# Performance work log

Measured on AMD Instinct MI355X. Metric: run time of the kernel, lower is better.

## Reference

```python
import jax, jax.numpy as jnp
import numpy as np

N = 50000      # nodes
E = 800000     # edges (avg degree 16)
IN, H, C = 128, 256, 47


def _linear_init(key, nin, nout):
    bound = 1.0 / np.sqrt(nin)
    kw, kb = jax.random.split(key)
    w = jax.random.uniform(kw, (nin, nout), jnp.float32, -bound, bound)
    b = jax.random.uniform(kb, (nout,), jnp.float32, -bound, bound)
    return w, b


def setup_inputs() -> dict:
    key = jax.random.key(0)
    ks = jax.random.split(key, 9)
    x = jax.random.normal(ks[0], (N, IN), jnp.float32)
    row = jax.random.randint(ks[1], (E,), 0, N)   # dst node of each edge
    col = jax.random.randint(ks[2], (E,), 0, N)   # src node of each edge
    y = jax.random.randint(ks[3], (N,), 0, C)
    train_mask = jax.random.randint(ks[4], (N,), 0, 2).astype(jnp.bool_)
    w1n, b1n = _linear_init(ks[5], IN, H)
    w1s, b1s = _linear_init(ks[6], IN, H)
    w2n, b2n = _linear_init(ks[7], H, C)
    w2s, b2s = _linear_init(ks[8], H, C)
    return {"x": x, "row": row, "col": col, "y": y, "train_mask": train_mask,
            "w1n": w1n, "b1n": b1n, "w1s": w1s, "b1s": b1s,
            "w2n": w2n, "b2n": b2n, "w2s": w2s, "b2s": b2s}


def _mean_aggr(h, row, col):
    # sparse adjacency matmul with reduce='mean': gather src feats, scatter-mean to dst
    s = jax.ops.segment_sum(h[col], row, num_segments=N)          # [N, d]
    deg = jax.ops.segment_sum(jnp.ones((E,), h.dtype), row, num_segments=N)
    return jnp.where(deg[:, None] > 0, s / jnp.maximum(deg, 1.0)[:, None], 0.0)


def reference(x, row, col, y, train_mask,
              w1n, b1n, w1s, b1s, w2n, b2n, w2s, b2s):
    # dropout in eval mode -> identity
    h = x
    # layer 1: SAGE = linear(mean_aggr(h)) + linear(h), then ReLU
    a = _mean_aggr(h, row, col)
    h1 = jax.nn.relu((a @ w1n + b1n) + (h @ w1s + b1s))           # [N, H]
    # layer 2 (output): SAGE then log_softmax
    a2 = _mean_aggr(h1, row, col)
    logits = (a2 @ w2n + b2n) + (h1 @ w2s + b2s)                  # [N, C]
    logp = jax.nn.log_softmax(logits, axis=1)
    nll = -jnp.take_along_axis(logp, y[:, None], axis=1)[:, 0]    # [N]
    m = train_mask.astype(logits.dtype)
    # nll_loss mean over train nodes; single chunk -> loss / num_chunks == loss
    loss = jnp.sum(nll * m) / jnp.maximum(jnp.sum(m), 1.0)
    return loss
```

## Files before the change

### kernel.cpp

```cpp
#include <hip/hip_runtime.h>
#include <math.h>

#define NN 50000
#define EE 800000
#define DIN 128
#define HH 256
#define CC 47
#define LK2 264
#define GS_BLOCKS 2048

typedef short bf16x8 __attribute__((ext_vector_type(8)));
typedef float f32x4 __attribute__((ext_vector_type(4)));
typedef float f32x2 __attribute__((ext_vector_type(2)));

static __device__ __forceinline__ unsigned short f2bf(float f) {
    unsigned u = __float_as_uint(f);
    u = u + 0x7fff + ((u >> 16) & 1);
    return (unsigned short)(u >> 16);
}
static __device__ __forceinline__ float bflo(unsigned u) { return __uint_as_float(u << 16); }
static __device__ __forceinline__ float bfhi(unsigned u) { return __uint_as_float(u & 0xffff0000u); }

__global__ __launch_bounds__(256) void prep_kernel(
    const float* __restrict__ x, const int* __restrict__ row,
    const int* __restrict__ col, const int* __restrict__ msk,
    const float* __restrict__ w1n, const float* __restrict__ w1s,
    const float* __restrict__ b1n, const float* __restrict__ b1s,
    const float* __restrict__ w2n, const float* __restrict__ w2s,
    int* __restrict__ cnt, unsigned short* __restrict__ bucket,
    unsigned* __restrict__ xq, unsigned* __restrict__ ab,
    unsigned short* __restrict__ WB1, unsigned short* __restrict__ WB2,
    float* __restrict__ bias1, int* __restrict__ mcount, int* __restrict__ mlist)
{
    int t = blockIdx.x * 256 + threadIdx.x;
    if (t < EE) {
        int r = row[t];
        int pos = atomicAdd(&cnt[r], 1);
        if (pos < 64) bucket[r * 64 + pos] = (unsigned short)col[t];
    }
    if (t < NN && msk[t]) {
        int p = atomicAdd(mcount, 1);
        mlist[p] = t;
    }
    if (t < NN * 32) {
        int i = t >> 5, c = t & 31;
        float4 v = *(const float4*)&x[(size_t)i * DIN + c * 4];
        int p = __builtin_amdgcn_cvt_pk_fp8_f32(v.x, v.y, 0, false);
        p = __builtin_amdgcn_cvt_pk_fp8_f32(v.z, v.w, p, true);
        xq[(size_t)i * 32 + c] = (unsigned)p;
        ab[(size_t)i * 128 + 64 + 2 * c]     = (unsigned)f2bf(v.x) | ((unsigned)f2bf(v.y) << 16);
        ab[(size_t)i * 128 + 64 + 2 * c + 1] = (unsigned)f2bf(v.z) | ((unsigned)f2bf(v.w) << 16);
    }
    if (t < 65536) {
        int k = t >> 8, n = t & 255;
        float v = (k < 128) ? w1n[k * HH + n] : w1s[(k - 128) * HH + n];
        WB1[n * 256 + k] = f2bf(v);
    } else if (t < 65536 + 24576) {
        int q = t - 65536;
        int k = q / 96, n = q % 96;
        float v;
        if (n < 48) v = (n < CC) ? w2n[k * CC + n] : 0.f;
        else { int m = n - 48; v = (m < CC) ? w2s[k * CC + m] : 0.f; }
        WB2[n * 256 + k] = f2bf(v);
    } else if (t < 65536 + 24576 + 256) {
        int n = t - 65536 - 24576;
        bias1[n] = b1n[n] + b1s[n];
    }
}

__global__ __launch_bounds__(256) void agg1(const unsigned* __restrict__ xq,
                                            const int* __restrict__ cnt,
                                            const unsigned short* __restrict__ bucket,
                                            unsigned* __restrict__ ab,
                                            float* __restrict__ inv) {
    int wave = threadIdx.x >> 6, lane = threadIdx.x & 63;
    const int h = lane >> 5, hl = lane & 31;
    const int W = gridDim.x * 4;
    for (int i = blockIdx.x * 4 + wave; i < NN; i += W) {
        int e = cnt[i];
        float dvs = fmaxf((float)e, 1.0f);
        if (e > 64) e = 64;
        float A0=0,A1=0,A2=0,A3=0, B0=0,B1=0,B2=0,B3=0;
        float C0=0,C1=0,C2=0,C3=0, D0=0,D1=0,D2=0,D3=0;
        if (e > 0) {
            int myidx = bucket[i * 64 + min(lane, e - 1)];
            int j = 0;
            for (; j + 16 <= e; j += 16) {
                int n0 = __shfl(myidx, j + h);
                int n1 = __shfl(myidx, j + 2 + h);
                int n2 = __shfl(myidx, j + 4 + h);
                int n3 = __shfl(myidx, j + 6 + h);
                int n4 = __shfl(myidx, j + 8 + h);
                int n5 = __shfl(myidx, j + 10 + h);
                int n6 = __shfl(myidx, j + 12 + h);
                int n7 = __shfl(myidx, j + 14 + h);
                unsigned u0 = xq[(size_t)n0 * 32 + hl];
                unsigned u1 = xq[(size_t)n1 * 32 + hl];
                unsigned u2 = xq[(size_t)n2 * 32 + hl];
                unsigned u3 = xq[(size_t)n3 * 32 + hl];
                unsigned u4 = xq[(size_t)n4 * 32 + hl];
                unsigned u5 = xq[(size_t)n5 * 32 + hl];
                unsigned u6 = xq[(size_t)n6 * 32 + hl];
                unsigned u7 = xq[(size_t)n7 * 32 + hl];
                f32x2 l0 = __builtin_amdgcn_cvt_pk_f32_fp8(u0, false);
                f32x2 h0 = __builtin_amdgcn_cvt_pk_f32_fp8(u0, true);
                f32x2 l1 = __builtin_amdgcn_cvt_pk_f32_fp8(u1, false);
                f32x2 h1 = __builtin_amdgcn_cvt_pk_f32_fp8(u1, true);
                f32x2 l2 = __builtin_amdgcn_cvt_pk_f32_fp8(u2, false);
                f32x2 h2 = __builtin_amdgcn_cvt_pk_f32_fp8(u2, true);
                f32x2 l3 = __builtin_amdgcn_cvt_pk_f32_fp8(u3, false);
                f32x2 h3 = __builtin_amdgcn_cvt_pk_f32_fp8(u3, true);
                A0 += l0.x; A1 += l0.y; A2 += h0.x; A3 += h0.y;
                B0 += l1.x; B1 += l1.y; B2 += h1.x; B3 += h1.y;
                C0 += l2.x; C1 += l2.y; C2 += h2.x; C3 += h2.y;
                D0 += l3.x; D1 += l3.y; D2 += h3.x; D3 += h3.y;
                f32x2 l4 = __builtin_amdgcn_cvt_pk_f32_fp8(u4, false);
                f32x2 h4 = __builtin_amdgcn_cvt_pk_f32_fp8(u4, true);
                f32x2 l5 = __builtin_amdgcn_cvt_pk_f32_fp8(u5, false);
                f32x2 h5 = __builtin_amdgcn_cvt_pk_f32_fp8(u5, true);
                f32x2 l6 = __builtin_amdgcn_cvt_pk_f32_fp8(u6, false);
                f32x2 h6 = __builtin_amdgcn_cvt_pk_f32_fp8(u6, true);
                f32x2 l7 = __builtin_amdgcn_cvt_pk_f32_fp8(u7, false);
                f32x2 h7 = __builtin_amdgcn_cvt_pk_f32_fp8(u7, true);
                A0 += l4.x; A1 += l4.y; A2 += h4.x; A3 += h4.y;
                B0 += l5.x; B1 += l5.y; B2 += h5.x; B3 += h5.y;
                C0 += l6.x; C1 += l6.y; C2 += h6.x; C3 += h6.y;
                D0 += l7.x; D1 += l7.y; D2 += h7.x; D3 += h7.y;
            }
            for (; j + 8 <= e; j += 8) {
                int n0 = __shfl(myidx, j + h);
                int n1 = __shfl(myidx, j + 2 + h);
                int n2 = __shfl(myidx, j + 4 + h);
                int n3 = __shfl(myidx, j + 6 + h);
                unsigned u0 = xq[(size_t)n0 * 32 + hl];
                unsigned u1 = xq[(size_t)n1 * 32 + hl];
                unsigned u2 = xq[(size_t)n2 * 32 + hl];
                unsigned u3 = xq[(size_t)n3 * 32 + hl];
                f32x2 l0 = __builtin_amdgcn_cvt_pk_f32_fp8(u0, false);
                f32x2 h0 = __builtin_amdgcn_cvt_pk_f32_fp8(u0, true);
                f32x2 l1 = __builtin_amdgcn_cvt_pk_f32_fp8(u1, false);
                f32x2 h1 = __builtin_amdgcn_cvt_pk_f32_fp8(u1, true);
                f32x2 l2 = __builtin_amdgcn_cvt_pk_f32_fp8(u2, false);
                f32x2 h2 = __builtin_amdgcn_cvt_pk_f32_fp8(u2, true);
                f32x2 l3 = __builtin_amdgcn_cvt_pk_f32_fp8(u3, false);
                f32x2 h3 = __builtin_amdgcn_cvt_pk_f32_fp8(u3, true);
                A0 += l0.x; A1 += l0.y; A2 += h0.x; A3 += h0.y;
                B0 += l1.x; B1 += l1.y; B2 += h1.x; B3 += h1.y;
                C0 += l2.x; C1 += l2.y; C2 += h2.x; C3 += h2.y;
                D0 += l3.x; D1 += l3.y; D2 += h3.x; D3 += h3.y;
            }
            for (; j < e; j += 2) {
                int src = j + h;
                int n = __shfl(myidx, min(src, e - 1));
                unsigned u = xq[(size_t)n * 32 + hl];
                if (src >= e) u = 0u;
                f32x2 lo = __builtin_amdgcn_cvt_pk_f32_fp8(u, false);
                f32x2 hi = __builtin_amdgcn_cvt_pk_f32_fp8(u, true);
                A0 += lo.x; A1 += lo.y; A2 += hi.x; A3 += hi.y;
            }
        }
        float s0 = (A0 + B0) + (C0 + D0);
        float s1 = (A1 + B1) + (C1 + D1);
        float s2 = (A2 + B2) + (C2 + D2);
        float s3 = (A3 + B3) + (C3 + D3);
        s0 += __shfl_xor(s0, 32); s1 += __shfl_xor(s1, 32);
        s2 += __shfl_xor(s2, 32); s3 += __shfl_xor(s3, 32);
        if (h == 0) {
            float sc = 1.0f / dvs;
            if (hl == 0) inv[i] = sc;
            unsigned d0 = (unsigned)f2bf(s0 * sc) | ((unsigned)f2bf(s1 * sc) << 16);
            unsigned d1 = (unsigned)f2bf(s2 * sc) | ((unsigned)f2bf(s3 * sc) << 16);
            *(uint2*)&ab[(size_t)i * 128 + 2 * hl] = make_uint2(d0, d1);
        }
    }
}

__global__ __launch_bounds__(256) void gemm12_fused(
    const unsigned short* __restrict__ AB,
    const unsigned short* __restrict__ WB1, const unsigned short* __restrict__ WB2,
    const float* __restrict__ bias1,
    const float* __restrict__ b2n, const float* __restrict__ b2s,
    unsigned* __restrict__ znb, float* __restrict__ zsb)
{
    __shared__ unsigned short sA[32 * LK2];
    __shared__ unsigned short sB[32 * LK2];
    __shared__ unsigned short sH[32 * LK2];
    const int tid = threadIdx.x;
    const int i0 = blockIdx.x * 32;
    const int wv = tid >> 6, lane = tid & 63;
    const int g = lane >> 4, l16 = lane & 15;
    const int m0 = (wv & 1) * 16, q0 = (wv >> 1) * 16;

#pragma unroll
    for (int l = 0; l < 4; ++l) {
        int c = tid + l * 256;
        int r = c >> 5, c8 = (c & 31) * 8;
        int gi = i0 + r;
        int4 v = make_int4(0, 0, 0, 0);
        if (gi < NN) v = *(const int4*)&AB[(size_t)gi * 256 + c8];
        *(int4*)&sA[r * LK2 + c8] = v;
    }

    for (int n0 = 0; n0 < 8; ++n0) {
#pragma unroll
        for (int l = 0; l < 4; ++l) {
            int c = tid + l * 256;
            int r = c >> 5, c8 = (c & 31) * 8;
            *(int4*)&sB[r * LK2 + c8] = *(const int4*)&WB1[(size_t)(n0 * 32 + r) * 256 + c8];
        }
        __syncthreads();
        f32x4 p0 = {}, p1 = {}, p2 = {}, p3 = {};
        {
            const unsigned short* ar = &sA[(m0 + l16) * LK2 + g * 8];
            const unsigned short* br = &sB[(q0 + l16) * LK2 + g * 8];
            p0 = __builtin_amdgcn_mfma_f32_16x16x32_bf16(*(const bf16x8*)(ar +   0), *(const bf16x8*)(br +   0), p0, 0, 0, 0);
            p1 = __builtin_amdgcn_mfma_f32_16x16x32_bf16(*(const bf16x8*)(ar +  32), *(const bf16x8*)(br +  32), p1, 0, 0, 0);
            p2 = __builtin_amdgcn_mfma_f32_16x16x32_bf16(*(const bf16x8*)(ar +  64), *(const bf16x8*)(br +  64), p2, 0, 0, 0);
            p3 = __builtin_amdgcn_mfma_f32_16x16x32_bf16(*(const bf16x8*)(ar +  96), *(const bf16x8*)(br +  96), p3, 0, 0, 0);
            p0 = __builtin_amdgcn_mfma_f32_16x16x32_bf16(*(const bf16x8*)(ar + 128), *(const bf16x8*)(br + 128), p0, 0, 0, 0);
            p1 = __builtin_amdgcn_mfma_f32_16x16x32_bf16(*(const bf16x8*)(ar + 160), *(const bf16x8*)(br + 160), p1, 0, 0, 0);
            p2 = __builtin_amdgcn_mfma_f32_16x16x32_bf16(*(const bf16x8*)(ar + 192), *(const bf16x8*)(br + 192), p2, 0, 0, 0);
            p3 = __builtin_amdgcn_mfma_f32_16x16x32_bf16(*(const bf16x8*)(ar + 224), *(const bf16x8*)(br + 224), p3, 0, 0, 0);
        }
        f32x4 acc = (p0 + p1) + (p2 + p3);
        int colh = n0 * 32 + q0 + l16;
        float bi = bias1[colh];
#pragma unroll
        for (int r = 0; r < 4; ++r)
            sH[(m0 + g * 4 + r) * LK2 + colh] = f2bf(fmaxf(acc[r] + bi, 0.f));
        __syncthreads();
    }

    for (int m = 0; m < 3; ++m) {
#pragma unroll
        for (int l = 0; l < 4; ++l) {
            int c = tid + l * 256;
            int r = c >> 5, c8 = (c & 31) * 8;
            *(int4*)&sB[r * LK2 + c8] = *(const int4*)&WB2[(size_t)(m * 32 + r) * 256 + c8];
        }
        __syncthreads();
        f32x4 p0 = {}, p1 = {}, p2 = {}, p3 = {};
        {
            const unsigned short* ar = &sH[(m0 + l16) * LK2 + g * 8];
            const unsigned short* br = &sB[(q0 + l16) * LK2 + g * 8];
            p0 = __builtin_amdgcn_mfma_f32_16x16x32_bf16(*(const bf16x8*)(ar +   0), *(const bf16x8*)(br +   0), p0, 0, 0, 0);
            p1 = __builtin_amdgcn_mfma_f32_16x16x32_bf16(*(const bf16x8*)(ar +  32), *(const bf16x8*)(br +  32), p1, 0, 0, 0);
            p2 = __builtin_amdgcn_mfma_f32_16x16x32_bf16(*(const bf16x8*)(ar +  64), *(const bf16x8*)(br +  64), p2, 0, 0, 0);
            p3 = __builtin_amdgcn_mfma_f32_16x16x32_bf16(*(const bf16x8*)(ar +  96), *(const bf16x8*)(br +  96), p3, 0, 0, 0);
            p0 = __builtin_amdgcn_mfma_f32_16x16x32_bf16(*(const bf16x8*)(ar + 128), *(const bf16x8*)(br + 128), p0, 0, 0, 0);
            p1 = __builtin_amdgcn_mfma_f32_16x16x32_bf16(*(const bf16x8*)(ar + 160), *(const bf16x8*)(br + 160), p1, 0, 0, 0);
            p2 = __builtin_amdgcn_mfma_f32_16x16x32_bf16(*(const bf16x8*)(ar + 192), *(const bf16x8*)(br + 192), p2, 0, 0, 0);
            p3 = __builtin_amdgcn_mfma_f32_16x16x32_bf16(*(const bf16x8*)(ar + 224), *(const bf16x8*)(br + 224), p3, 0, 0, 0);
        }
        f32x4 acc = (p0 + p1) + (p2 + p3);
        int c = m * 32 + q0 + l16;
        if (c < 48) {
#pragma unroll
            for (int r = 0; r < 4; ++r) {
                int gi = i0 + m0 + g * 4 + r;
                float v = acc[r];
                float vp = __shfl_down(v, 1);
                if (((l16 & 1) == 0) && gi < NN)
                    znb[(size_t)gi * 24 + (c >> 1)] =
                        (unsigned)f2bf(v) | ((unsigned)f2bf(vp) << 16);
            }
        } else {
            int cz = c - 48;
            float bias = (cz < CC) ? (b2n[cz] + b2s[cz]) : 0.f;
#pragma unroll
            for (int r = 0; r < 4; ++r) {
                int gi = i0 + m0 + g * 4 + r;
                if (gi < NN) zsb[(size_t)gi * 48 + cz] = acc[r] + bias;
            }
        }
        __syncthreads();
    }
}

__global__ __launch_bounds__(256) void loss_kernel(
    const unsigned* __restrict__ znb, const float* __restrict__ zsb,
    const int* __restrict__ cnt, const unsigned short* __restrict__ bucket,
    const float* __restrict__ inv, const int* __restrict__ y,
    const int* __restrict__ mcount, const int* __restrict__ mlist,
    float* __restrict__ accum)
{
    __shared__ float red[16];
    const int tid = threadIdx.x;
    const int wave = tid >> 6, lane = tid & 63;
    const int half = lane >> 5, hl = lane & 31;
    const int h32 = lane & 32;
    const bool act = hl < 24;
    const int dw = act ? hl : 0;
    const int W = gridDim.x * 8;
    const int M = mcount[0];
    float num = 0.f, den = 0.f;

    for (int p = (blockIdx.x * 4 + wave) * 2 + half; p < M; p += W) {
        int i = mlist[p];
        int e = cnt[i];
        if (e > 64) e = 64;
        float plo[8] = {}, phi[8] = {};
        for (int base = 0; base < e; base += 32) {
            int c2 = min(32, e - base);
            int myidx = bucket[i * 64 + min(base + hl, e - 1)];
            int j = 0;
            for (; j + 8 <= c2; j += 8) {
                unsigned uu[8];
#pragma unroll
                for (int k = 0; k < 8; ++k) {
                    int n = __shfl(myidx, h32 + j + k);
                    uu[k] = znb[(size_t)n * 24 + dw];
                }
#pragma unroll
                for (int k = 0; k < 8; ++k) {
                    plo[k] += bflo(uu[k]); phi[k] += bfhi(uu[k]);
                }
            }
            for (; j + 4 <= c2; j += 4) {
                unsigned uu[4];
#pragma unroll
                for (int k = 0; k < 4; ++k) {
                    int n = __shfl(myidx, h32 + j + k);
                    uu[k] = znb[(size_t)n * 24 + dw];
                }
#pragma unroll
                for (int k = 0; k < 4; ++k) {
                    plo[k] += bflo(uu[k]); phi[k] += bfhi(uu[k]);
                }
            }
            for (; j < c2; ++j) {
                int n = __shfl(myidx, h32 + j);
                unsigned u = znb[(size_t)n * 24 + dw];
                plo[0] += bflo(u); phi[0] += bfhi(u);
            }
        }
        float alo = ((plo[0] + plo[1]) + (plo[2] + plo[3])) +
                    ((plo[4] + plo[5]) + (plo[6] + plo[7]));
        float ahi = ((phi[0] + phi[1]) + (phi[2] + phi[3])) +
                    ((phi[4] + phi[5]) + (phi[6] + phi[7]));

        float sc = inv[i];
        float llo = -1e30f, lhi = -1e30f;
        if (act) {
            float2 zs = *(const float2*)&zsb[(size_t)i * 48 + 2 * hl];
            llo = alo * sc + zs.x;
            lhi = ahi * sc + zs.y;
        }
        if (hl == 23) lhi = -1e30f;
        float mx = fmaxf(llo, lhi);
#pragma unroll
        for (int off = 16; off >= 1; off >>= 1)
            mx = fmaxf(mx, __shfl_xor(mx, off));
        float sm = act ? (__expf(llo - mx) + __expf(lhi - mx)) : 0.f;
#pragma unroll
        for (int off = 16; off >= 1; off >>= 1)
            sm += __shfl_xor(sm, off);
        float lse = mx + __logf(sm);
        int yi = y[i];
        float gl = __shfl(llo, h32 + (yi >> 1));
        float gh = __shfl(lhi, h32 + (yi >> 1));
        float ly = (yi & 1) ? gh : gl;
        if (hl == 0) { num += lse - ly; den += 1.f; }
    }
    if (hl == 0) {
        red[wave * 4 + half * 2]     = num;
        red[wave * 4 + half * 2 + 1] = den;
    }
    __syncthreads();
    if (tid == 0) {
        float n = 0.f, d = 0.f;
#pragma unroll
        for (int k = 0; k < 16; k += 2) { n += red[k]; d += red[k + 1]; }
        atomicAdd(&accum[0], n);
        atomicAdd(&accum[1], d);
    }
}

__global__ void finalize_kernel(const float* __restrict__ accum, float* __restrict__ out) {
    out[0] = accum[0] / fmaxf(accum[1], 1.0f);
}

extern "C" void kernel_launch(void* const* d_in, const int* in_sizes, int n_in,
                              void* d_out, int out_size, void* d_ws, size_t ws_size,
                              hipStream_t stream) {
    const float* x   = (const float*)d_in[0];
    const int*   row = (const int*)d_in[1];
    const int*   col = (const int*)d_in[2];
    const int*   y   = (const int*)d_in[3];
    const int*   msk = (const int*)d_in[4];
    const float* w1n = (const float*)d_in[5];
    const float* b1n = (const float*)d_in[6];
    const float* w1s = (const float*)d_in[7];
    const float* b1s = (const float*)d_in[8];
    const float* w2n = (const float*)d_in[9];
    const float* b2n = (const float*)d_in[10];
    const float* w2s = (const float*)d_in[11];
    const float* b2s = (const float*)d_in[12];
    float* out = (float*)d_out;

    float* ws      = (float*)d_ws;
    float* accum   = ws;
    int*   mcount  = (int*)(ws + 32);
    int*   cnt     = (int*)(ws + 64);
    unsigned short* bucket = (unsigned short*)(cnt + 50048);
    unsigned* xq   = (unsigned*)(bucket + 3200000);
    unsigned* ab   = xq + (size_t)NN * 32;
    unsigned* znb  = ab + (size_t)NN * 128;
    float* zsb     = (float*)(znb + (size_t)NN * 24);
    unsigned short* WB1 = (unsigned short*)(zsb + (size_t)NN * 48);
    unsigned short* WB2 = WB1 + 65536;
    float* bias1   = (float*)(WB2 + 24576);
    int*   mlist   = (int*)(bias1 + 256);
    float* inv     = (float*)(mlist + 50048);

    (void)hipMemsetAsync(accum, 0, (64 + 50048) * sizeof(float), stream);

    prep_kernel<<<(NN * 32 + 255) / 256, 256, 0, stream>>>(
        x, row, col, msk, w1n, w1s, b1n, b1s, w2n, w2s,
        cnt, bucket, xq, ab, WB1, WB2, bias1, mcount, mlist);

    agg1<<<GS_BLOCKS, 256, 0, stream>>>(xq, cnt, bucket, ab, inv);

    gemm12_fused<<<(NN + 31) / 32, 256, 0, stream>>>(
        (const unsigned short*)ab, WB1, WB2, bias1, b2n, b2s, znb, zsb);

    loss_kernel<<<GS_BLOCKS, 256, 0, stream>>>(
        znb, zsb, cnt, bucket, inv, y, mcount, mlist, accum);

    finalize_kernel<<<1, 1, 0, stream>>>(accum, out);
}
```

Baseline: 255.2 us.

## Store layer-2 neighbor logits in fp8 and restructure loss gather per node pairs

The layer-2 neighbor projection is stored as fp8 (16 dwords per node, 64 bytes) instead of bf16 (24 dwords), which shrinks the gather traffic in the loss kernel. The loss kernel now has each half-wave process two fixed consecutive nodes and check the mask inline, dropping the atomic-built masked node list and the stored inverse-degree array. Each half-wave splits into two edge groups of 16 lanes, each lane handling four classes, with a cross-group shuffle reduction. The cost is fp8 rounding error in the aggregated logits, plus idle work on unmasked nodes.

```diff
diff --git a/kernel.cpp b/kernel.cpp
--- a/kernel.cpp
+++ b/kernel.cpp
@@ -8,6 +8,7 @@
 #define CC 47
 #define LK2 264
 #define GS_BLOCKS 2048
+#define LOSS_BLOCKS 3136
 
 typedef short bf16x8 __attribute__((ext_vector_type(8)));
 typedef float f32x4 __attribute__((ext_vector_type(4)));
@@ -18,19 +19,17 @@
     u = u + 0x7fff + ((u >> 16) & 1);
     return (unsigned short)(u >> 16);
 }
-static __device__ __forceinline__ float bflo(unsigned u) { return __uint_as_float(u << 16); }
-static __device__ __forceinline__ float bfhi(unsigned u) { return __uint_as_float(u & 0xffff0000u); }
 
 __global__ __launch_bounds__(256) void prep_kernel(
     const float* __restrict__ x, const int* __restrict__ row,
-    const int* __restrict__ col, const int* __restrict__ msk,
+    const int* __restrict__ col,
     const float* __restrict__ w1n, const float* __restrict__ w1s,
     const float* __restrict__ b1n, const float* __restrict__ b1s,
     const float* __restrict__ w2n, const float* __restrict__ w2s,
     int* __restrict__ cnt, unsigned short* __restrict__ bucket,
     unsigned* __restrict__ xq, unsigned* __restrict__ ab,
     unsigned short* __restrict__ WB1, unsigned short* __restrict__ WB2,
-    float* __restrict__ bias1, int* __restrict__ mcount, int* __restrict__ mlist)
+    float* __restrict__ bias1, unsigned* __restrict__ znq)
 {
     int t = blockIdx.x * 256 + threadIdx.x;
     if (t < EE) {
@@ -38,9 +37,8 @@
         int pos = atomicAdd(&cnt[r], 1);
         if (pos < 64) bucket[r * 64 + pos] = (unsigned short)col[t];
     }
-    if (t < NN && msk[t]) {
-        int p = atomicAdd(mcount, 1);
-        mlist[p] = t;
+    if (t < NN) {
+        *(uint4*)&znq[(size_t)t * 16 + 12] = make_uint4(0u, 0u, 0u, 0u);
     }
     if (t < NN * 32) {
         int i = t >> 5, c = t & 31;
@@ -71,8 +69,7 @@
 __global__ __launch_bounds__(256) void agg1(const unsigned* __restrict__ xq,
                                             const int* __restrict__ cnt,
                                             const unsigned short* __restrict__ bucket,
-                                            unsigned* __restrict__ ab,
-                                            float* __restrict__ inv) {
+                                            unsigned* __restrict__ ab) {
     int wave = threadIdx.x >> 6, lane = threadIdx.x & 63;
     const int h = lane >> 5, hl = lane & 31;
     const int W = gridDim.x * 4;
@@ -167,7 +164,6 @@
         s2 += __shfl_xor(s2, 32); s3 += __shfl_xor(s3, 32);
         if (h == 0) {
             float sc = 1.0f / dvs;
-            if (hl == 0) inv[i] = sc;
             unsigned d0 = (unsigned)f2bf(s0 * sc) | ((unsigned)f2bf(s1 * sc) << 16);
             unsigned d1 = (unsigned)f2bf(s2 * sc) | ((unsigned)f2bf(s3 * sc) << 16);
             *(uint2*)&ab[(size_t)i * 128 + 2 * hl] = make_uint2(d0, d1);
@@ -180,7 +176,7 @@
     const unsigned short* __restrict__ WB1, const unsigned short* __restrict__ WB2,
     const float* __restrict__ bias1,
     const float* __restrict__ b2n, const float* __restrict__ b2s,
-    unsigned* __restrict__ znb, float* __restrict__ zsb)
+    unsigned* __restrict__ znq, float* __restrict__ zsb)
 {
     __shared__ unsigned short sA[32 * LK2];
     __shared__ unsigned short sB[32 * LK2];
@@ -259,10 +255,14 @@
             for (int r = 0; r < 4; ++r) {
                 int gi = i0 + m0 + g * 4 + r;
                 float v = acc[r];
-                float vp = __shfl_down(v, 1);
-                if (((l16 & 1) == 0) && gi < NN)
-                    znb[(size_t)gi * 24 + (c >> 1)] =
-                        (unsigned)f2bf(v) | ((unsigned)f2bf(vp) << 16);
+                float v1 = __shfl_down(v, 1);
+                float v2 = __shfl_down(v, 2);
+                float v3 = __shfl_down(v, 3);
+                if (((l16 & 3) == 0) && gi < NN) {
+                    int pk = __builtin_amdgcn_cvt_pk_fp8_f32(v, v1, 0, false);
+                    pk = __builtin_amdgcn_cvt_pk_fp8_f32(v2, v3, pk, true);
+                    znq[(size_t)gi * 16 + (c >> 2)] = (unsigned)pk;
+                }
             }
         } else {
             int cz = c - 48;
@@ -278,10 +278,9 @@
 }
 
 __global__ __launch_bounds__(256) void loss_kernel(
-    const unsigned* __restrict__ znb, const float* __restrict__ zsb,
-    const int* __restrict__ cnt, const unsigned short* __restrict__ bucket,
-    const float* __restrict__ inv, const int* __restrict__ y,
-    const int* __restrict__ mcount, const int* __restrict__ mlist,
+    const unsigned* __restrict__ znq, const float* __restrict__ zsb,
+    const int* __restrict__ msk, const int* __restrict__ cnt,
+    const unsigned short* __restrict__ bucket, const int* __restrict__ y,
     float* __restrict__ accum)
 {
     __shared__ float red[16];
@@ -289,79 +288,112 @@
     const int wave = tid >> 6, lane = tid & 63;
     const int half = lane >> 5, hl = lane & 31;
     const int h32 = lane & 32;
-    const bool act = hl < 24;
-    const int dw = act ? hl : 0;
-    const int W = gridDim.x * 8;
-    const int M = mcount[0];
+    const int eg = hl >> 4, dwl = hl & 15;
+    const int hw = (blockIdx.x * 4 + wave) * 2 + half;
+    const int base = hw * 2;
     float num = 0.f, den = 0.f;
 
-    for (int p = (blockIdx.x * 4 + wave) * 2 + half; p < M; p += W) {
-        int i = mlist[p];
-        int e = cnt[i];
-        if (e > 64) e = 64;
-        float plo[8] = {}, phi[8] = {};
-        for (int base = 0; base < e; base += 32) {
-            int c2 = min(32, e - base);
-            int myidx = bucket[i * 64 + min(base + hl, e - 1)];
+    int mk2 = 0, c2v = 0, y2 = 0;
+    if (hl < 2 && base + hl < NN) {
+        mk2 = msk[base + hl];
+        c2v = cnt[base + hl];
+        y2  = y[base + hl];
+    }
+    int midx[2];
+#pragma unroll
+    for (int k = 0; k < 2; ++k) {
+        int mkk = __shfl(mk2, h32 + k);
+        int ck  = __shfl(c2v, h32 + k);
+        int ek  = min(ck, 64);
+        midx[k] = 0;
+        if (mkk && ek > 0)
+            midx[k] = bucket[(size_t)(base + k) * 64 + min(hl, ek - 1)];
+    }
+
+#pragma unroll
+    for (int k = 0; k < 2; ++k) {
+        int i = base + k;
+        if (i >= NN) break;
+        int mkk = __shfl(mk2, h32 + k);
+        if (!mkk) continue;
+        int c = __shfl(c2v, h32 + k);
+        int e = min(c, 64);
+        float sc = 1.0f / fmaxf((float)c, 1.0f);
+
+        int dwm = min(dwl, 11);
+        float4 zs = *(const float4*)&zsb[(size_t)i * 48 + 4 * dwm];
+
+        float p0 = 0.f, p1 = 0.f, p2 = 0.f, p3 = 0.f;
+        int mi = midx[k];
+        for (int b = 0; b < e; b += 32) {
+            int cc = min(32, e - b);
+            if (b) mi = bucket[(size_t)i * 64 + min(b + hl, e - 1)];
             int j = 0;
-            for (; j + 8 <= c2; j += 8) {
+            for (; j + 16 <= cc; j += 16) {
                 unsigned uu[8];
 #pragma unroll
-                for (int k = 0; k < 8; ++k) {
-                    int n = __shfl(myidx, h32 + j + k);
-                    uu[k] = znb[(size_t)n * 24 + dw];
+                for (int q = 0; q < 8; ++q) {
+                    int n = __shfl(mi, h32 + j + 2 * q + eg);
+                    uu[q] = znq[(size_t)n * 16 + dwl];
                 }
 #pragma unroll
-                for (int k = 0; k < 8; ++k) {
-                    plo[k] += bflo(uu[k]); phi[k] += bfhi(uu[k]);
+                for (int q = 0; q < 8; ++q) {
+                    f32x2 lo = __builtin_amdgcn_cvt_pk_f32_fp8(uu[q], false);
+                    f32x2 hi = __builtin_amdgcn_cvt_pk_f32_fp8(uu[q], true);
+                    p0 += lo.x; p1 += lo.y; p2 += hi.x; p3 += hi.y;
                 }
             }
-            for (; j + 4 <= c2; j += 4) {
+            for (; j + 8 <= cc; j += 8) {
                 unsigned uu[4];
 #pragma unroll
-                for (int k = 0; k < 4; ++k) {
-                    int n = __shfl(myidx, h32 + j + k);
-                    uu[k] = znb[(size_t)n * 24 + dw];
+                for (int q = 0; q < 4; ++q) {
+                    int n = __shfl(mi, h32 + j + 2 * q + eg);
+                    uu[q] = znq[(size_t)n * 16 + dwl];
                 }
 #pragma unroll
-                for (int k = 0; k < 4; ++k) {
-                    plo[k] += bflo(uu[k]); phi[k] += bfhi(uu[k]);
+                for (int q = 0; q < 4; ++q) {
+                    f32x2 lo = __builtin_amdgcn_cvt_pk_f32_fp8(uu[q], false);
+                    f32x2 hi = __builtin_amdgcn_cvt_pk_f32_fp8(uu[q], true);
+                    p0 += lo.x; p1 += lo.y; p2 += hi.x; p3 += hi.y;
                 }
             }
-            for (; j < c2; ++j) {
-                int n = __shfl(myidx, h32 + j);
-                unsigned u = znb[(size_t)n * 24 + dw];
-                plo[0] += bflo(u); phi[0] += bfhi(u);
-            }
-        }
-        float alo = ((plo[0] + plo[1]) + (plo[2] + plo[3])) +
-                    ((plo[4] + plo[5]) + (plo[6] + plo[7]));
-        float ahi = ((phi[0] + phi[1]) + (phi[2] + phi[3])) +
-                    ((phi[4] + phi[5]) + (phi[6] + phi[7]));
-
-        float sc = inv[i];
-        float llo = -1e30f, lhi = -1e30f;
-        if (act) {
-            float2 zs = *(const float2*)&zsb[(size_t)i * 48 + 2 * hl];
-            llo = alo * sc + zs.x;
-            lhi = ahi * sc + zs.y;
-        }
-        if (hl == 23) lhi = -1e30f;
-        float mx = fmaxf(llo, lhi);
-#pragma unroll
-        for (int off = 16; off >= 1; off >>= 1)
+            for (; j < cc; j += 2) {
+                int src = j + eg;
+                int n = __shfl(mi, h32 + min(src, cc - 1));
+                unsigned u = znq[(size_t)n * 16 + dwl];
+                if (src >= cc) u = 0u;
+                f32x2 lo = __builtin_amdgcn_cvt_pk_f32_fp8(u, false);
+                f32x2 hi = __builtin_amdgcn_cvt_pk_f32_fp8(u, true);
+                p0 += lo.x; p1 += lo.y; p2 += hi.x; p3 += hi.y;
+            }
+        }
+        p0 += __shfl_xor(p0, 16); p1 += __shfl_xor(p1, 16);
+        p2 += __shfl_xor(p2, 16); p3 += __shfl_xor(p3, 16);
+
+        float l0 = -1e30f, l1 = -1e30f, l2 = -1e30f, l3 = -1e30f;
+        if (dwl < 12) {
+            l0 = p0 * sc + zs.x;
+            l1 = p1 * sc + zs.y;
+            l2 = p2 * sc + zs.z;
+            l3 = (dwl == 11) ? -1e30f : (p3 * sc + zs.w);
+        }
+        float mx = fmaxf(fmaxf(l0, l1), fmaxf(l2, l3));
+#pragma unroll
+        for (int off = 8; off >= 1; off >>= 1)
             mx = fmaxf(mx, __shfl_xor(mx, off));
-        float sm = act ? (__expf(llo - mx) + __expf(lhi - mx)) : 0.f;
-#pragma unroll
-        for (int off = 16; off >= 1; off >>= 1)
+        float sm = __expf(l0 - mx) + __expf(l1 - mx) +
+                   __expf(l2 - mx) + __expf(l3 - mx);
+#pragma unroll
+        for (int off = 8; off >= 1; off >>= 1)
             sm += __shfl_xor(sm, off);
         float lse = mx + __logf(sm);
-        int yi = y[i];
-        float gl = __shfl(llo, h32 + (yi >> 1));
-        float gh = __shfl(lhi, h32 + (yi >> 1));
-        float ly = (yi & 1) ? gh : gl;
+
+        int yi = __shfl(y2, h32 + k);
+        float vsel = (yi & 2) ? ((yi & 1) ? l3 : l2) : ((yi & 1) ? l1 : l0);
+        float ly = __shfl(vsel, h32 + (yi >> 2));
         if (hl == 0) { num += lse - ly; den += 1.f; }
     }
+
     if (hl == 0) {
         red[wave * 4 + half * 2]     = num;
         red[wave * 4 + half * 2 + 1] = den;
@@ -400,32 +432,29 @@
 
     float* ws      = (float*)d_ws;
     float* accum   = ws;
-    int*   mcount  = (int*)(ws + 32);
     int*   cnt     = (int*)(ws + 64);
     unsigned short* bucket = (unsigned short*)(cnt + 50048);
     unsigned* xq   = (unsigned*)(bucket + 3200000);
     unsigned* ab   = xq + (size_t)NN * 32;
-    unsigned* znb  = ab + (size_t)NN * 128;
-    float* zsb     = (float*)(znb + (size_t)NN * 24);
+    unsigned* znq  = ab + (size_t)NN * 128;
+    float* zsb     = (float*)(znq + (size_t)NN * 16);
     unsigned short* WB1 = (unsigned short*)(zsb + (size_t)NN * 48);
     unsigned short* WB2 = WB1 + 65536;
     float* bias1   = (float*)(WB2 + 24576);
-    int*   mlist   = (int*)(bias1 + 256);
-    float* inv     = (float*)(mlist + 50048);
 
     (void)hipMemsetAsync(accum, 0, (64 + 50048) * sizeof(float), stream);
 
     prep_kernel<<<(NN * 32 + 255) / 256, 256, 0, stream>>>(
-        x, row, col, msk, w1n, w1s, b1n, b1s, w2n, w2s,
-        cnt, bucket, xq, ab, WB1, WB2, bias1, mcount, mlist);
-
-    agg1<<<GS_BLOCKS, 256, 0, stream>>>(xq, cnt, bucket, ab, inv);
+        x, row, col, w1n, w1s, b1n, b1s, w2n, w2s,
+        cnt, bucket, xq, ab, WB1, WB2, bias1, znq);
+
+    agg1<<<GS_BLOCKS, 256, 0, stream>>>(xq, cnt, bucket, ab);
 
     gemm12_fused<<<(NN + 31) / 32, 256, 0, stream>>>(
-        (const unsigned short*)ab, WB1, WB2, bias1, b2n, b2s, znb, zsb);
-
-    loss_kernel<<<GS_BLOCKS, 256, 0, stream>>>(
-        znb, zsb, cnt, bucket, inv, y, mcount, mlist, accum);
+        (const unsigned short*)ab, WB1, WB2, bias1, b2n, b2s, znq, zsb);
+
+    loss_kernel<<<LOSS_BLOCKS, 256, 0, stream>>>(
+        znq, zsb, msk, cnt, bucket, y, accum);
 
     finalize_kernel<<<1, 1, 0, stream>>>(accum, out);
 }
```

New measurement: 283.3 us. +11.0%, slower.
